# Optimization experiments

Hardware: AMD Instinct MI355X
Metric: run time of the kernel (lower is better)

## Reference

```python
import jax, jax.numpy as jnp
import numpy as np

LEAK = 0.2
N, C, T, H, DOUT = 512, 16, 15, 32, 32


def setup_inputs() -> dict:
    key = jax.random.key(0)
    k = jax.random.split(key, 5)
    x = jax.random.normal(k[0], (N, C), dtype=jnp.float32)
    adj = jax.random.uniform(k[1], (N, N, T), dtype=jnp.float32)
    W1 = jax.random.normal(k[2], (2 * C, T + 1, H), dtype=jnp.float32) * 0.05
    W2 = jax.random.normal(k[3], (2 * C, T + 1, DOUT), dtype=jnp.float32) * 0.05
    W3 = jax.random.normal(k[4], (C, H), dtype=jnp.float32) * 0.05
    return {"x": x, "adj": adj, "W1": W1, "W2": W2, "W3": W3}


def reference(x, adj, W1, W2, W3):
    n, c = x.shape
    # input_diag: [N,N,C,1], diagonal copy of node features
    diag = jnp.einsum('mn,ni->mni', jnp.eye(n, dtype=x.dtype), x)[..., None]
    # D = concat(adj-weighted broadcast of x, diag) along edge-type axis -> [N,N,C,T+1]
    D = jnp.concatenate([jnp.einsum('mnt,ni->mnit', adj, x), diag], axis=3)
    # symmetrize along channel axis -> [N,N,2C,T+1]
    D = jnp.concatenate([D, jnp.transpose(D, (1, 0, 2, 3))], axis=2)
    K = jnp.einsum('mnit,ith->mnh', D, W1)   # [N,N,H]
    V = jnp.einsum('mnit,itd->mnd', D, W2)   # [N,N,DOUT]
    Q = x @ W3                               # [N,H]
    logits1 = jnp.einsum('nh,nmh->nm', Q, K)
    logits2 = jnp.einsum('mh,nmh->nm', Q, K)
    s1 = jax.nn.softmax(logits1, axis=1)
    s2 = jax.nn.softmax(logits2, axis=0)
    temp = jnp.einsum('nm,nmd->nd', s1, V) + jnp.einsum('nm,nmd->md', s2, V)
    return jnp.maximum(temp, LEAK * temp)  # lrelu
```

## Files before the change

### kernel.cpp

```cpp
#include <hip/hip_runtime.h>
#include <hip/hip_bf16.h>

#define NNODE 512
#define CCH   16
#define TT    15
#define TP    16
#define HH    32
#define DD    32

typedef unsigned short u16;
typedef unsigned int   u32;
typedef short bf8 __attribute__((ext_vector_type(8)));
typedef float f4  __attribute__((ext_vector_type(4)));

__device__ __forceinline__ float bf2f(u16 v) {
    union { u32 u; float f; } x; x.u = ((u32)v) << 16; return x.f;
}
__device__ __forceinline__ u16 f2bf(float f) {
    union { float f; u32 u; } x; x.f = f;
    u32 u = x.u;
    return (u16)((u + 0x7FFFu + ((u >> 16) & 1u)) >> 16);
}
__device__ __forceinline__ void unpack8(uint4 p, float* o) {
    o[0]=bf2f((u16)(p.x & 0xffffu)); o[1]=bf2f((u16)(p.x >> 16));
    o[2]=bf2f((u16)(p.y & 0xffffu)); o[3]=bf2f((u16)(p.y >> 16));
    o[4]=bf2f((u16)(p.z & 0xffffu)); o[5]=bf2f((u16)(p.z >> 16));
    o[6]=bf2f((u16)(p.w & 0xffffu)); o[7]=bf2f((u16)(p.w >> 16));
}
__device__ __forceinline__ uint4 pack8(const u16* v) {
    return make_uint4((u32)v[0]|((u32)v[1]<<16), (u32)v[2]|((u32)v[3]<<16),
                      (u32)v[4]|((u32)v[5]<<16), (u32)v[6]|((u32)v[7]<<16));
}

__global__ __launch_bounds__(256) void k_prep_adjp(
    const float* __restrict__ x, const float* __restrict__ W1,
    const float* __restrict__ W2, const float* __restrict__ W3,
    const float* __restrict__ adj,
    u16* __restrict__ A1, u16* __restrict__ B1,
    u16* __restrict__ A2T, u16* __restrict__ B2T,
    u16* __restrict__ Qb, float* __restrict__ QAd, float* __restrict__ QB,
    u16* __restrict__ adjP, u16* __restrict__ adjPT)
{
    int tid = threadIdx.x;
    if (blockIdx.x < 512) {
        int n = blockIdx.x;
        __shared__ alignas(16) float xs[CCH];
        __shared__ alignas(16) float A1row[512], B1row[512];
        __shared__ alignas(16) float A2row[512], B2row[512];
        __shared__ alignas(16) float Qs[HH];
        if (tid < CCH) xs[tid] = x[n*CCH + tid];
        __syncthreads();
        float xr[CCH];
        #pragma unroll
        for (int i=0;i<CCH;i++) xr[i]=xs[i];
        #pragma unroll
        for (int rep=0; rep<2; rep++) {
            int c = tid + rep*256;
            float a1=0.f,b1=0.f,a2=0.f,b2=0.f;
            #pragma unroll
            for (int i=0;i<CCH;i++) {
                a1 += xr[i]*W1[i*512 + c];
                b1 += xr[i]*W1[(CCH+i)*512 + c];
                a2 += xr[i]*W2[i*512 + c];
                b2 += xr[i]*W2[(CCH+i)*512 + c];
            }
            A1[(size_t)n*512 + c]=f2bf(a1); B1[(size_t)n*512 + c]=f2bf(b1);
            A1row[c]=a1; B1row[c]=b1; A2row[c]=a2; B2row[c]=b2;
        }
        if (tid < HH) {
            float q=0.f;
            #pragma unroll
            for (int i=0;i<CCH;i++) q += xr[i]*W3[i*HH + tid];
            Qs[tid]=q; Qb[(size_t)n*HH + tid]=f2bf(q);
        }
        __syncthreads();
        if (tid < TP) {
            float qa=0.f, qb=0.f;
            #pragma unroll
            for (int h=0;h<HH;h++) { qa += Qs[h]*A1row[tid*HH+h]; qb += Qs[h]*B1row[tid*HH+h]; }
            QAd[(size_t)n*TP + tid]=qa; QB[(size_t)n*TP + tid]=qb;
        }
        {
            int d = tid >> 3, t0 = (tid & 7) * 2;
            u32 pa = (u32)f2bf(A2row[t0*32 + d]) | ((u32)f2bf(A2row[(t0+1)*32 + d]) << 16);
            u32 pb = (u32)f2bf(B2row[t0*32 + d]) | ((u32)f2bf(B2row[(t0+1)*32 + d]) << 16);
            *(u32*)(A2T + (size_t)d*8192 + n*16 + t0) = pa;
            *(u32*)(B2T + (size_t)d*8192 + n*16 + t0) = pb;
        }
    } else {
        int b = blockIdx.x - 512;
        int n0 = (b >> 4) * 32, m0 = (b & 15) * 32;
        __shared__ alignas(16) u16 s[32*520];
        #pragma unroll
        for (int i = 0; i < 60; i++) {
            int e = tid + i*256;
            int nl = e / 480; int rem = e - nl*480;
            int ml = rem / 15; int t = rem - ml*15;
            float v = adj[((size_t)(n0+nl)*512 + (m0+ml))*TT + t];
            s[nl*520 + ml*16 + t] = f2bf(v);
        }
        #pragma unroll
        for (int i = 0; i < 4; i++) {
            int e = tid + i*256; int nl = e >> 5, ml = e & 31;
            s[nl*520 + ml*16 + 15] = ((n0+nl) == (m0+ml)) ? (u16)0x3F80 : (u16)0;
        }
        __syncthreads();
        #pragma unroll
        for (int i = 0; i < 8; i++) {
            int c = tid + i*256;
            int nl = c >> 6, off = (c & 63) * 8;
            uint4 vv = *(const uint4*)(s + nl*520 + off);
            *(uint4*)(adjP + (size_t)(n0+nl)*8192 + m0*16 + off) = vv;
        }
        #pragma unroll
        for (int i = 0; i < 8; i++) {
            int c = tid + i*256;
            int ml = c >> 6, nlh = c & 63, nl = nlh >> 1, half = nlh & 1;
            uint4 vv = *(const uint4*)(s + nl*520 + ml*16 + half*8);
            *(uint4*)(adjPT + (size_t)(m0+ml)*8192 + (n0+nl)*16 + half*8) = vv;
        }
    }
}

__global__ __launch_bounds__(256) void k_logits(
    const u16* __restrict__ Qb, const u16* __restrict__ A1, const u16* __restrict__ B1,
    const u16* __restrict__ adjP, const u16* __restrict__ adjPT,
    const float* __restrict__ QAd, const float* __restrict__ QB,
    float* __restrict__ L1, float* __restrict__ L2T)
{
    const int m0 = blockIdx.x * 16, n0 = blockIdx.y * 16;
    const int tid = threadIdx.x;
    const int wv = tid >> 6, lane = tid & 63, l15 = lane & 15, quad = lane >> 4;
    __shared__ alignas(16) float sL1[16*17];
    __shared__ alignas(16) float sL2[16*17];

    bf8 qbN = *(const bf8*)(Qb + (size_t)(n0 + l15)*32 + quad*8);
    bf8 qbM = *(const bf8*)(Qb + (size_t)(m0 + l15)*32 + quad*8);
    float4 qb4 = *(const float4*)(QB  + (size_t)(n0 + l15)*TP + quad*4);
    float4 qa4 = *(const float4*)(QAd + (size_t)(m0 + l15)*TP + quad*4);

    #pragma unroll
    for (int j = 0; j < 4; j++) {
        int m = m0 + wv*4 + j;
        bf8 aA1 = *(const bf8*)(A1 + (size_t)m*512 + l15*32 + quad*8);
        f4 z = {0.f,0.f,0.f,0.f};
        f4 g = __builtin_amdgcn_mfma_f32_16x16x32_bf16(aA1, qbN, z, 0, 0, 0);
        uint2 ax = *(const uint2*)(adjPT + (size_t)m*8192 + (n0 + l15)*16 + quad*4);
        uint2 ay = *(const uint2*)(adjP  + (size_t)m*8192 + (n0 + l15)*16 + quad*4);
        float v;
        v = bf2f((u16)(ax.x & 0xffffu)) * g[0];
        v = fmaf(bf2f((u16)(ax.x >> 16)),     g[1], v);
        v = fmaf(bf2f((u16)(ax.y & 0xffffu)), g[2], v);
        v = fmaf(bf2f((u16)(ax.y >> 16)),     g[3], v);
        v = fmaf(bf2f((u16)(ay.x & 0xffffu)), qb4.x, v);
        v = fmaf(bf2f((u16)(ay.x >> 16)),     qb4.y, v);
        v = fmaf(bf2f((u16)(ay.y & 0xffffu)), qb4.z, v);
        v = fmaf(bf2f((u16)(ay.y >> 16)),     qb4.w, v);
        v += __shfl_xor(v, 16, 64);
        v += __shfl_xor(v, 32, 64);
        if (quad == 0) sL1[l15*17 + wv*4 + j] = v;
    }
    #pragma unroll
    for (int j = 0; j < 4; j++) {
        int n = n0 + wv*4 + j;
        bf8 aB1 = *(const bf8*)(B1 + (size_t)n*512 + l15*32 + quad*8);
        f4 z = {0.f,0.f,0.f,0.f};
        f4 h = __builtin_amdgcn_mfma_f32_16x16x32_bf16(aB1, qbM, z, 0, 0, 0);
        uint2 ax = *(const uint2*)(adjPT + (size_t)n*8192 + (m0 + l15)*16 + quad*4);
        uint2 ay = *(const uint2*)(adjP  + (size_t)n*8192 + (m0 + l15)*16 + quad*4);
        float v;
        v = bf2f((u16)(ax.x & 0xffffu)) * h[0];
        v = fmaf(bf2f((u16)(ax.x >> 16)),     h[1], v);
        v = fmaf(bf2f((u16)(ax.y & 0xffffu)), h[2], v);
        v = fmaf(bf2f((u16)(ax.y >> 16)),     h[3], v);
        v = fmaf(bf2f((u16)(ay.x & 0xffffu)), qa4.x, v);
        v = fmaf(bf2f((u16)(ay.x >> 16)),     qa4.y, v);
        v = fmaf(bf2f((u16)(ay.y & 0xffffu)), qa4.z, v);
        v = fmaf(bf2f((u16)(ay.y >> 16)),     qa4.w, v);
        v += __shfl_xor(v, 16, 64);
        v += __shfl_xor(v, 32, 64);
        if (quad == 0) sL2[l15*17 + wv*4 + j] = v;
    }
    __syncthreads();
    int row = tid >> 4, col = tid & 15;
    L1 [(size_t)(n0+row)*NNODE + m0 + col] = sL1[row*17+col];
    L2T[(size_t)(m0+row)*NNODE + n0 + col] = sL2[row*17+col];
}

__global__ __launch_bounds__(256) void k_softmax_w(
    const float* __restrict__ L1, const float* __restrict__ L2T,
    const u16* __restrict__ adjP, const u16* __restrict__ adjPT,
    u16* __restrict__ W1c, u16* __restrict__ W2c,
    float* __restrict__ u1, float* __restrict__ v2)
{
    int b = blockIdx.x, tid = threadIdx.x;
    bool first = b < NNODE;
    int j = first ? b : b - NNODE;
    const float* row = first ? (L1 + (size_t)j*NNODE) : (L2T + (size_t)j*NNODE);
    u16* W  = (first ? W1c : W2c) + (size_t)j*8192;
    float* uv = (first ? u1 : v2) + (size_t)j*TP;

    float v0 = row[tid], v1 = row[tid+256];
    float mx = fmaxf(v0, v1);
    #pragma unroll
    for (int o=32; o; o>>=1) mx = fmaxf(mx, __shfl_xor(mx, o, 64));
    __shared__ alignas(16) float red[4], red2[4], ur[4][16];
    int lane = tid & 63, wv = tid >> 6;
    if (!lane) red[wv] = mx;
    __syncthreads();
    mx = fmaxf(fmaxf(red[0],red[1]), fmaxf(red[2],red[3]));
    float e0 = __expf(v0 - mx), e1 = __expf(v1 - mx);
    float sm = e0 + e1;
    #pragma unroll
    for (int o=32; o; o>>=1) sm += __shfl_xor(sm, o, 64);
    if (!lane) red2[wv] = sm;
    __syncthreads();
    float inv = 1.0f / (red2[0]+red2[1]+red2[2]+red2[3]);
    float sa = e0*inv, sb = e1*inv;

    const u16* ap = adjP  + (size_t)j*8192;
    const u16* tp = adjPT + (size_t)j*8192;
    float u[16];
    #pragma unroll
    for (int t=0;t<16;t++) u[t]=0.f;
    #pragma unroll
    for (int half = 0; half < 2; half++) {
        int k = tid + half*256;
        float sv = half ? sb : sa;
        const uint4* p = (const uint4*)(ap + k*16);
        float av[16]; unpack8(p[0], av); unpack8(p[1], av+8);
        u16 o16[16];
        #pragma unroll
        for (int t=0;t<16;t++) o16[t] = f2bf(sv*av[t]);
        uint4* wp = (uint4*)(W + k*16);
        wp[0] = pack8(o16); wp[1] = pack8(o16+8);
        const uint4* q = (const uint4*)(tp + k*16);
        float tv[16]; unpack8(q[0], tv); unpack8(q[1], tv+8);
        #pragma unroll
        for (int t=0;t<16;t++) u[t] = fmaf(sv, tv[t], u[t]);
    }
    #pragma unroll
    for (int i=0;i<8;i++) {
        float s0 = (lane&1) ? u[i] : u[i+8];
        float r0 = __shfl_xor(s0, 1, 64);
        u[i] = ((lane&1) ? u[i+8] : u[i]) + r0;
    }
    #pragma unroll
    for (int i=0;i<4;i++) {
        float s0 = (lane&2) ? u[i] : u[i+4];
        float r0 = __shfl_xor(s0, 2, 64);
        u[i] = ((lane&2) ? u[i+4] : u[i]) + r0;
    }
    #pragma unroll
    for (int i=0;i<2;i++) {
        float s0 = (lane&4) ? u[i] : u[i+2];
        float r0 = __shfl_xor(s0, 4, 64);
        u[i] = ((lane&4) ? u[i+2] : u[i]) + r0;
    }
    {
        float s0 = (lane&8) ? u[0] : u[1];
        float r0 = __shfl_xor(s0, 8, 64);
        u[0] = ((lane&8) ? u[1] : u[0]) + r0;
    }
    u[0] += __shfl_xor(u[0], 16, 64);
    u[0] += __shfl_xor(u[0], 32, 64);
    if (lane < 16) {
        int tm = ((lane&1)<<3) | ((lane&2)<<1) | ((lane&4)>>1) | ((lane&8)>>3);
        ur[wv][tm] = u[0];
    }
    __syncthreads();
    if (tid < 16) uv[tid] = ur[0][tid]+ur[1][tid]+ur[2][tid]+ur[3][tid];
}

__global__ __launch_bounds__(256) void k_gemm2(
    const u16* __restrict__ W1c, const u16* __restrict__ W2c,
    const u16* __restrict__ A2T, const u16* __restrict__ B2T,
    float* __restrict__ tempP)
{
    int tid = threadIdx.x;
    int wv = tid >> 6, lane = tid & 63, l15 = lane & 15, quad = lane >> 4;
    int w = blockIdx.x*4 + wv;
    int kc = w & 15, dt = (w >> 4) & 1, jt = w >> 5;
    size_t aRow = (size_t)(jt*16 + l15)*8192;
    size_t bRow = (size_t)(dt*16 + l15)*8192;
    int kt0 = kc*512 + quad*8;
    f4 acc = {0.f, 0.f, 0.f, 0.f};
    #pragma unroll
    for (int s = 0; s < 16; s++) {
        int kt = kt0 + s*32;
        bf8 aw1 = *(const bf8*)(W1c + aRow + kt);
        bf8 ba2 = *(const bf8*)(A2T + bRow + kt);
        acc = __builtin_amdgcn_mfma_f32_16x16x32_bf16(aw1, ba2, acc, 0, 0, 0);
        bf8 aw2 = *(const bf8*)(W2c + aRow + kt);
        bf8 bb2 = *(const bf8*)(B2T + bRow + kt);
        acc = __builtin_amdgcn_mfma_f32_16x16x32_bf16(aw2, bb2, acc, 0, 0, 0);
    }
    #pragma unroll
    for (int r = 0; r < 4; r++)
        tempP[((size_t)kc*NNODE + jt*16 + quad*4 + r)*DD + dt*16 + l15] = acc[r];
}

__global__ __launch_bounds__(256) void k_final(
    const float* __restrict__ tempP, const float* __restrict__ u1, const float* __restrict__ v2,
    const u16* __restrict__ A2T, const u16* __restrict__ B2T, float* __restrict__ out)
{
    int base = blockIdx.x * 256 + threadIdx.x;
    int j = base >> 5, d = base & 31;
    float acc = 0.f;
    #pragma unroll
    for (int kc=0;kc<16;kc++) acc += tempP[((size_t)kc*NNODE + j)*DD + d];
    const uint4* pb2 = (const uint4*)(B2T + (size_t)d*8192 + j*16);
    const uint4* pa2 = (const uint4*)(A2T + (size_t)d*8192 + j*16);
    float bv[16], av[16];
    unpack8(pb2[0], bv); unpack8(pb2[1], bv+8);
    unpack8(pa2[0], av); unpack8(pa2[1], av+8);
    #pragma unroll
    for (int t = 0; t < 16; t++)
        acc += u1[(size_t)j*TP + t]*bv[t] + v2[(size_t)j*TP + t]*av[t];
    out[(size_t)j*DD + d] = fmaxf(acc, 0.2f*acc);
}

extern "C" void kernel_launch(void* const* d_in, const int* in_sizes, int n_in,
                              void* d_out, int out_size, void* d_ws, size_t ws_size,
                              hipStream_t stream)
{
    (void)in_sizes; (void)n_in; (void)out_size; (void)ws_size;
    const float* x   = (const float*)d_in[0];
    const float* adj = (const float*)d_in[1];
    const float* W1  = (const float*)d_in[2];
    const float* W2  = (const float*)d_in[3];
    const float* W3  = (const float*)d_in[4];

    char* ws = (char*)d_ws;
    u16*   adjP = (u16*)(ws);
    u16*   adjPT= (u16*)(ws + 0x800000);
    u16*   W1c  = (u16*)(ws + 0x1000000);
    u16*   W2c  = (u16*)(ws + 0x1800000);
    u16*   A1   = (u16*)(ws + 0x2000000);
    u16*   B1   = (u16*)(ws + 0x2080000);
    u16*   A2T  = (u16*)(ws + 0x2100000);
    u16*   B2T  = (u16*)(ws + 0x2180000);
    u16*   Qb   = (u16*)(ws + 0x2200000);
    float* QAd  = (float*)(ws + 0x2210000);
    float* QB   = (float*)(ws + 0x2220000);
    float* u1   = (float*)(ws + 0x2230000);
    float* v2   = (float*)(ws + 0x2240000);
    float* L1   = (float*)(ws + 0x2300000);
    float* L2T  = (float*)(ws + 0x2400000);
    float* tempP= (float*)(ws + 0x2500000);

    k_prep_adjp<<<768, 256, 0, stream>>>(x, W1, W2, W3, adj,
                                         A1, B1, A2T, B2T, Qb, QAd, QB, adjP, adjPT);
    k_logits<<<dim3(32,32), 256, 0, stream>>>(Qb, A1, B1, adjP, adjPT, QAd, QB, L1, L2T);
    k_softmax_w<<<1024, 256, 0, stream>>>(L1, L2T, adjP, adjPT, W1c, W2c, u1, v2);
    k_gemm2<<<256, 256, 0, stream>>>(W1c, W2c, A2T, B2T, tempP);
    k_final<<<64, 256, 0, stream>>>(tempP, u1, v2, A2T, B2T, (float*)d_out);
}
```

Baseline: 106.8 us.

## Fuse softmax weighting with second GEMM via LDS-staged weighted adjacency tiles

Merges the softmax/weight-scaling kernel and the second MFMA GEMM into one kernel. Each block recomputes row softmax statistics for 16 rows, builds the scaled bf16 weight tile in swizzled shared memory, and feeds it straight into MFMAs. This removes the 16 MB global write and read of the W1c/W2c intermediates and one kernel launch. In exchange, softmax max/sum is recomputed redundantly across the 16 k-chunks, and partial u and temp sums go to global for k_final to reduce over 32 partials.

After: 103.4 us. 3.1% less time.

```diff
diff --git a/kernel.cpp b/kernel.cpp
--- a/kernel.cpp
+++ b/kernel.cpp
@@ -187,136 +187,154 @@
     L2T[(size_t)(m0+row)*NNODE + n0 + col] = sL2[row*17+col];
 }
 
-__global__ __launch_bounds__(256) void k_softmax_w(
+__global__ __launch_bounds__(256) void k_smx_gemm(
     const float* __restrict__ L1, const float* __restrict__ L2T,
     const u16* __restrict__ adjP, const u16* __restrict__ adjPT,
-    u16* __restrict__ W1c, u16* __restrict__ W2c,
-    float* __restrict__ u1, float* __restrict__ v2)
-{
-    int b = blockIdx.x, tid = threadIdx.x;
-    bool first = b < NNODE;
-    int j = first ? b : b - NNODE;
-    const float* row = first ? (L1 + (size_t)j*NNODE) : (L2T + (size_t)j*NNODE);
-    u16* W  = (first ? W1c : W2c) + (size_t)j*8192;
-    float* uv = (first ? u1 : v2) + (size_t)j*TP;
-
-    float v0 = row[tid], v1 = row[tid+256];
-    float mx = fmaxf(v0, v1);
-    #pragma unroll
-    for (int o=32; o; o>>=1) mx = fmaxf(mx, __shfl_xor(mx, o, 64));
-    __shared__ alignas(16) float red[4], red2[4], ur[4][16];
-    int lane = tid & 63, wv = tid >> 6;
-    if (!lane) red[wv] = mx;
-    __syncthreads();
-    mx = fmaxf(fmaxf(red[0],red[1]), fmaxf(red[2],red[3]));
-    float e0 = __expf(v0 - mx), e1 = __expf(v1 - mx);
-    float sm = e0 + e1;
-    #pragma unroll
-    for (int o=32; o; o>>=1) sm += __shfl_xor(sm, o, 64);
-    if (!lane) red2[wv] = sm;
-    __syncthreads();
-    float inv = 1.0f / (red2[0]+red2[1]+red2[2]+red2[3]);
-    float sa = e0*inv, sb = e1*inv;
-
-    const u16* ap = adjP  + (size_t)j*8192;
-    const u16* tp = adjPT + (size_t)j*8192;
-    float u[16];
-    #pragma unroll
-    for (int t=0;t<16;t++) u[t]=0.f;
-    #pragma unroll
-    for (int half = 0; half < 2; half++) {
-        int k = tid + half*256;
-        float sv = half ? sb : sa;
-        const uint4* p = (const uint4*)(ap + k*16);
-        float av[16]; unpack8(p[0], av); unpack8(p[1], av+8);
-        u16 o16[16];
-        #pragma unroll
-        for (int t=0;t<16;t++) o16[t] = f2bf(sv*av[t]);
-        uint4* wp = (uint4*)(W + k*16);
-        wp[0] = pack8(o16); wp[1] = pack8(o16+8);
-        const uint4* q = (const uint4*)(tp + k*16);
-        float tv[16]; unpack8(q[0], tv); unpack8(q[1], tv+8);
-        #pragma unroll
-        for (int t=0;t<16;t++) u[t] = fmaf(sv, tv[t], u[t]);
-    }
-    #pragma unroll
-    for (int i=0;i<8;i++) {
-        float s0 = (lane&1) ? u[i] : u[i+8];
-        float r0 = __shfl_xor(s0, 1, 64);
-        u[i] = ((lane&1) ? u[i+8] : u[i]) + r0;
-    }
-    #pragma unroll
-    for (int i=0;i<4;i++) {
-        float s0 = (lane&2) ? u[i] : u[i+4];
-        float r0 = __shfl_xor(s0, 2, 64);
-        u[i] = ((lane&2) ? u[i+4] : u[i]) + r0;
-    }
-    #pragma unroll
-    for (int i=0;i<2;i++) {
-        float s0 = (lane&4) ? u[i] : u[i+2];
-        float r0 = __shfl_xor(s0, 4, 64);
-        u[i] = ((lane&4) ? u[i+2] : u[i]) + r0;
-    }
+    const u16* __restrict__ A2T, const u16* __restrict__ B2T,
+    float* __restrict__ tempP2, float* __restrict__ uP)
+{
+    const int j0 = blockIdx.x * 16, kc = blockIdx.y, dir = blockIdx.z;
+    const int tid = threadIdx.x;
+    const int wv = tid >> 6, lane = tid & 63, l15 = lane & 15, quad = lane >> 4;
+    const float* Lbase = dir ? L2T : L1;
+
+    __shared__ alignas(16) u16 Wt[16*512];
+    __shared__ alignas(16) float redb[4][512];
+    __shared__ float mxs[16], invs[16];
+
+    #pragma unroll
+    for (int rr = 0; rr < 4; rr++) {
+        int jr = wv*4 + rr;
+        const float* rw = Lbase + (size_t)(j0 + jr)*NNODE;
+        float4 a = *(const float4*)(rw + lane*8);
+        float4 b = *(const float4*)(rw + lane*8 + 4);
+        float mx = fmaxf(fmaxf(fmaxf(a.x,a.y),fmaxf(a.z,a.w)),
+                         fmaxf(fmaxf(b.x,b.y),fmaxf(b.z,b.w)));
+        #pragma unroll
+        for (int o=32; o; o>>=1) mx = fmaxf(mx, __shfl_xor(mx, o, 64));
+        float sm = __expf(a.x-mx)+__expf(a.y-mx)+__expf(a.z-mx)+__expf(a.w-mx)
+                 + __expf(b.x-mx)+__expf(b.y-mx)+__expf(b.z-mx)+__expf(b.w-mx);
+        #pragma unroll
+        for (int o=32; o; o>>=1) sm += __shfl_xor(sm, o, 64);
+        if (lane == 0) { mxs[jr] = mx; invs[jr] = 1.0f/sm; }
+    }
+    __syncthreads();
+
     {
-        float s0 = (lane&8) ? u[0] : u[1];
-        float r0 = __shfl_xor(s0, 8, 64);
-        u[0] = ((lane&8) ? u[1] : u[0]) + r0;
-    }
-    u[0] += __shfl_xor(u[0], 16, 64);
-    u[0] += __shfl_xor(u[0], 32, 64);
-    if (lane < 16) {
-        int tm = ((lane&1)<<3) | ((lane&2)<<1) | ((lane&4)>>1) | ((lane&8)>>3);
-        ur[wv][tm] = u[0];
-    }
-    __syncthreads();
-    if (tid < 16) uv[tid] = ur[0][tid]+ur[1][tid]+ur[2][tid]+ur[3][tid];
-}
-
-__global__ __launch_bounds__(256) void k_gemm2(
-    const u16* __restrict__ W1c, const u16* __restrict__ W2c,
-    const u16* __restrict__ A2T, const u16* __restrict__ B2T,
-    float* __restrict__ tempP)
-{
-    int tid = threadIdx.x;
-    int wv = tid >> 6, lane = tid & 63, l15 = lane & 15, quad = lane >> 4;
-    int w = blockIdx.x*4 + wv;
-    int kc = w & 15, dt = (w >> 4) & 1, jt = w >> 5;
-    size_t aRow = (size_t)(jt*16 + l15)*8192;
-    size_t bRow = (size_t)(dt*16 + l15)*8192;
-    int kt0 = kc*512 + quad*8;
-    f4 acc = {0.f, 0.f, 0.f, 0.f};
-    #pragma unroll
-    for (int s = 0; s < 16; s++) {
-        int kt = kt0 + s*32;
-        bf8 aw1 = *(const bf8*)(W1c + aRow + kt);
-        bf8 ba2 = *(const bf8*)(A2T + bRow + kt);
-        acc = __builtin_amdgcn_mfma_f32_16x16x32_bf16(aw1, ba2, acc, 0, 0, 0);
-        bf8 aw2 = *(const bf8*)(W2c + aRow + kt);
-        bf8 bb2 = *(const bf8*)(B2T + bRow + kt);
-        acc = __builtin_amdgcn_mfma_f32_16x16x32_bf16(aw2, bb2, acc, 0, 0, 0);
-    }
-    #pragma unroll
-    for (int r = 0; r < 4; r++)
-        tempP[((size_t)kc*NNODE + jt*16 + quad*4 + r)*DD + dt*16 + l15] = acc[r];
+        int j = tid >> 4, cb = tid & 15;
+        float mxj = mxs[j], invj = invs[j];
+        int mg = kc*32 + cb*2;
+        const float* rw = Lbase + (size_t)(j0 + j)*NNODE;
+        float s0 = __expf(rw[mg]   - mxj) * invj;
+        float s1 = __expf(rw[mg+1] - mxj) * invj;
+
+        const uint4* pp = (const uint4*)(adjP + (size_t)(j0+j)*8192 + kc*512 + cb*32);
+        float av[32];
+        unpack8(pp[0], av); unpack8(pp[1], av+8); unpack8(pp[2], av+16); unpack8(pp[3], av+24);
+        u16 wo[32];
+        #pragma unroll
+        for (int e=0;e<16;e++) wo[e]    = f2bf(s0*av[e]);
+        #pragma unroll
+        for (int e=0;e<16;e++) wo[16+e] = f2bf(s1*av[16+e]);
+        #pragma unroll
+        for (int q=0;q<4;q++) {
+            int sl = (cb*4 + q) ^ (j & 7);
+            *(uint4*)&Wt[j*512 + sl*8] = pack8(wo + q*8);
+        }
+
+        const uint4* qq4 = (const uint4*)(adjPT + (size_t)(j0+j)*8192 + kc*512 + cb*32);
+        float tv[32];
+        unpack8(qq4[0], tv); unpack8(qq4[1], tv+8); unpack8(qq4[2], tv+16); unpack8(qq4[3], tv+24);
+        float ut[16];
+        #pragma unroll
+        for (int t=0;t<16;t++) ut[t] = s0*tv[t] + s1*tv[16+t];
+        #pragma unroll
+        for (int i=0;i<8;i++) {
+            float v0 = (lane&1) ? ut[i] : ut[i+8];
+            float r0 = __shfl_xor(v0, 1, 64);
+            ut[i] = ((lane&1) ? ut[i+8] : ut[i]) + r0;
+        }
+        #pragma unroll
+        for (int i=0;i<4;i++) {
+            float v0 = (lane&2) ? ut[i] : ut[i+4];
+            float r0 = __shfl_xor(v0, 2, 64);
+            ut[i] = ((lane&2) ? ut[i+4] : ut[i]) + r0;
+        }
+        #pragma unroll
+        for (int i=0;i<2;i++) {
+            float v0 = (lane&4) ? ut[i] : ut[i+2];
+            float r0 = __shfl_xor(v0, 4, 64);
+            ut[i] = ((lane&4) ? ut[i+2] : ut[i]) + r0;
+        }
+        {
+            float v0 = (lane&8) ? ut[0] : ut[1];
+            float r0 = __shfl_xor(v0, 8, 64);
+            ut[0] = ((lane&8) ? ut[1] : ut[0]) + r0;
+        }
+        int tm = ((cb&1)<<3) | ((cb&2)<<1) | ((cb&4)>>1) | ((cb&8)>>3);
+        uP[((size_t)(dir*16 + kc)*NNODE + j0 + j)*TP + tm] = ut[0];
+    }
+    __syncthreads();
+
+    {
+        const u16* Bmat = dir ? B2T : A2T;
+        f4 acc0 = {0.f,0.f,0.f,0.f}, acc1 = {0.f,0.f,0.f,0.f};
+        #pragma unroll
+        for (int st = 0; st < 4; st++) {
+            int s = wv*4 + st;
+            bf8 afr = *(const bf8*)&Wt[l15*512 + (((s*4 + quad) ^ (l15 & 7)) << 3)];
+            bf8 b0 = *(const bf8*)(Bmat + (size_t)(l15)*8192    + kc*512 + s*32 + quad*8);
+            bf8 b1 = *(const bf8*)(Bmat + (size_t)(16+l15)*8192 + kc*512 + s*32 + quad*8);
+            acc0 = __builtin_amdgcn_mfma_f32_16x16x32_bf16(afr, b0, acc0, 0, 0, 0);
+            acc1 = __builtin_amdgcn_mfma_f32_16x16x32_bf16(afr, b1, acc1, 0, 0, 0);
+        }
+        #pragma unroll
+        for (int r = 0; r < 4; r++) {
+            redb[wv][      (quad*4+r)*16 + l15] = acc0[r];
+            redb[wv][256 + (quad*4+r)*16 + l15] = acc1[r];
+        }
+    }
+    __syncthreads();
+    #pragma unroll
+    for (int h = 0; h < 2; h++) {
+        int o = tid + h*256;
+        int jj = o >> 5, d = o & 31;
+        int idx = (d >> 4)*256 + jj*16 + (d & 15);
+        float v = redb[0][idx] + redb[1][idx] + redb[2][idx] + redb[3][idx];
+        tempP2[(((size_t)dir*16 + kc)*NNODE + j0 + jj)*DD + d] = v;
+    }
 }
 
 __global__ __launch_bounds__(256) void k_final(
-    const float* __restrict__ tempP, const float* __restrict__ u1, const float* __restrict__ v2,
+    const float* __restrict__ tempP2, const float* __restrict__ uP,
     const u16* __restrict__ A2T, const u16* __restrict__ B2T, float* __restrict__ out)
 {
-    int base = blockIdx.x * 256 + threadIdx.x;
-    int j = base >> 5, d = base & 31;
+    int blk = blockIdx.x, tid = threadIdx.x;
+    int jbase = blk*8;
+    __shared__ float u1L[8][16], v2L[8][16];
+    {
+        int dsel = tid >> 7;
+        int i = tid & 127; int jj = i >> 4, t = i & 15;
+        float s = 0.f;
+        #pragma unroll
+        for (int kcc = 0; kcc < 16; kcc++)
+            s += uP[(((size_t)dsel*16 + kcc)*NNODE + jbase + jj)*TP + t];
+        if (dsel) v2L[jj][t] = s; else u1L[jj][t] = s;
+    }
+    __syncthreads();
+    int base = blk*256 + tid;
+    int j = base >> 5, d = base & 31, jj = j & 7;
     float acc = 0.f;
     #pragma unroll
-    for (int kc=0;kc<16;kc++) acc += tempP[((size_t)kc*NNODE + j)*DD + d];
+    for (int p = 0; p < 32; p++) acc += tempP2[((size_t)p*NNODE + j)*DD + d];
     const uint4* pb2 = (const uint4*)(B2T + (size_t)d*8192 + j*16);
     const uint4* pa2 = (const uint4*)(A2T + (size_t)d*8192 + j*16);
-    float bv[16], av[16];
-    unpack8(pb2[0], bv); unpack8(pb2[1], bv+8);
-    unpack8(pa2[0], av); unpack8(pa2[1], av+8);
+    float bv[16], avv[16];
+    unpack8(pb2[0], bv);  unpack8(pb2[1], bv+8);
+    unpack8(pa2[0], avv); unpack8(pa2[1], avv+8);
     #pragma unroll
     for (int t = 0; t < 16; t++)
-        acc += u1[(size_t)j*TP + t]*bv[t] + v2[(size_t)j*TP + t]*av[t];
+        acc += u1L[jj][t]*bv[t] + v2L[jj][t]*avv[t];
     out[(size_t)j*DD + d] = fmaxf(acc, 0.2f*acc);
 }
 
@@ -332,27 +350,23 @@
     const float* W3  = (const float*)d_in[4];
 
     char* ws = (char*)d_ws;
-    u16*   adjP = (u16*)(ws);
-    u16*   adjPT= (u16*)(ws + 0x800000);
-    u16*   W1c  = (u16*)(ws + 0x1000000);
-    u16*   W2c  = (u16*)(ws + 0x1800000);
-    u16*   A1   = (u16*)(ws + 0x2000000);
-    u16*   B1   = (u16*)(ws + 0x2080000);
-    u16*   A2T  = (u16*)(ws + 0x2100000);
-    u16*   B2T  = (u16*)(ws + 0x2180000);
-    u16*   Qb   = (u16*)(ws + 0x2200000);
-    float* QAd  = (float*)(ws + 0x2210000);
-    float* QB   = (float*)(ws + 0x2220000);
-    float* u1   = (float*)(ws + 0x2230000);
-    float* v2   = (float*)(ws + 0x2240000);
-    float* L1   = (float*)(ws + 0x2300000);
-    float* L2T  = (float*)(ws + 0x2400000);
-    float* tempP= (float*)(ws + 0x2500000);
+    u16*   adjP  = (u16*)(ws);
+    u16*   adjPT = (u16*)(ws + 0x800000);
+    u16*   A1    = (u16*)(ws + 0x1000000);
+    u16*   B1    = (u16*)(ws + 0x1080000);
+    u16*   A2T   = (u16*)(ws + 0x1100000);
+    u16*   B2T   = (u16*)(ws + 0x1180000);
+    u16*   Qb    = (u16*)(ws + 0x1200000);
+    float* QAd   = (float*)(ws + 0x1210000);
+    float* QB    = (float*)(ws + 0x1220000);
+    float* L1    = (float*)(ws + 0x1300000);
+    float* L2T   = (float*)(ws + 0x1400000);
+    float* tempP2= (float*)(ws + 0x1500000);
+    float* uP    = (float*)(ws + 0x1700000);
 
     k_prep_adjp<<<768, 256, 0, stream>>>(x, W1, W2, W3, adj,
                                          A1, B1, A2T, B2T, Qb, QAd, QB, adjP, adjPT);
     k_logits<<<dim3(32,32), 256, 0, stream>>>(Qb, A1, B1, adjP, adjPT, QAd, QB, L1, L2T);
-    k_softmax_w<<<1024, 256, 0, stream>>>(L1, L2T, adjP, adjPT, W1c, W2c, u1, v2);
-    k_gemm2<<<256, 256, 0, stream>>>(W1c, W2c, A2T, B2T, tempP);
-    k_final<<<64, 256, 0, stream>>>(tempP, u1, v2, A2T, B2T, (float*)d_out);
-}
+    k_smx_gemm<<<dim3(32,16,2), 256, 0, stream>>>(L1, L2T, adjP, adjPT, A2T, B2T, tempP2, uP);
+    k_final<<<64, 256, 0, stream>>>(tempP2, uP, A2T, B2T, (float*)d_out);
+}
```
